# Kernel tuning notes

Measured on AMD Instinct MI355X. Metric: run time of the kernel, lower is better.

Reference implementation:

```python
import jax, jax.numpy as jnp
import numpy as np

HID = 1024
IN_DIM = 512
BATCH = 4096


def setup_inputs() -> dict:
    key = jax.random.key(0)
    ks = jax.random.split(key, 7)
    def lin(k, fan_in, fan_out):
        bound = 1.0 / np.sqrt(fan_in)
        kw, kb = jax.random.split(k)
        W = jax.random.uniform(kw, (fan_in, fan_out), jnp.float32, -bound, bound)
        b = jax.random.uniform(kb, (fan_out,), jnp.float32, -bound, bound)
        return W, b
    W_e, b_e = lin(ks[0], IN_DIM, HID)
    W_d, b_d = lin(ks[1], 4 * HID, HID)
    W_r, b_r = lin(ks[2], 3 * HID, 1)
    x = jax.random.normal(ks[3], (BATCH, IN_DIM), jnp.float32)
    return {"x": x, "W_e": W_e, "b_e": b_e, "W_d": W_d, "b_d": b_d,
            "W_r": W_r, "b_r": b_r, "steps": 12}


def reference(x, W_e, b_e, W_d, b_d, W_r, b_r, steps):
    # p: (B, h) embedded phases
    p = x @ W_e + b_e
    xp_c = jnp.cos(p)  # xp[:, :, 0]
    xp_s = jnp.sin(p)  # xp[:, :, 1]

    def step(ph, _):
        inp = jnp.concatenate([jnp.cos(ph), jnp.sin(ph), xp_c, xp_s], axis=1)  # (B, 4h)
        ph_new = ph + inp @ W_d + b_d
        return ph_new, ph_new

    ph0 = jnp.zeros((x.shape[0], W_e.shape[1]), dtype=x.dtype)
    ph, H = jax.lax.scan(step, ph0, None, length=steps)  # H: (steps, B, h)
    out = jnp.concatenate([jnp.cos(ph), jnp.sin(ph), ph], axis=1) @ W_r + b_r  # (B, 1)
    return out, H
```

## Files before the change

### kernel.cpp

```cpp
#include <hip/hip_runtime.h>
#include <hip/hip_bf16.h>
#include <math.h>

#define HID 1024
#define BATCH 4096
#define STEPS 12

typedef __attribute__((ext_vector_type(8))) short short8;
typedef __attribute__((ext_vector_type(4))) float f32x4;
typedef __attribute__((ext_vector_type(4))) unsigned short us4;
typedef unsigned short u16;

__device__ __forceinline__ u16 f2bf(float f) {
    union { float f; unsigned u; } v; v.f = f;
    unsigned r = v.u + 0x7fffu + ((v.u >> 16) & 1u);
    return (u16)(r >> 16);
}

__device__ __forceinline__ void gload_lds16(const u16* g, u16* l) {
    __builtin_amdgcn_global_load_lds(
        (const __attribute__((address_space(1))) unsigned*)g,
        (__attribute__((address_space(3))) unsigned*)l, 16, 0, 0);
}


__global__ void rm_convert_bf16(const float* __restrict__ in, u16* __restrict__ out, int n4) {
    int i = blockIdx.x * 256 + threadIdx.x;
    if (i >= n4) return;
    f32x4 v = *(const f32x4*)(in + (size_t)i * 4);
    us4 o;
    o[0] = f2bf(v[0]); o[1] = f2bf(v[1]); o[2] = f2bf(v[2]); o[3] = f2bf(v[3]);
    *(us4*)(out + (size_t)i * 4) = o;
}

__global__ void rm_transpose_bf16(const float* __restrict__ in, u16* __restrict__ out, int R, int C) {
    __shared__ float t[32][33];
    int c0 = blockIdx.x * 32, r0 = blockIdx.y * 32;
    int tx = threadIdx.x & 31, ty = threadIdx.x >> 5;
    #pragma unroll
    for (int i = 0; i < 32; i += 8)
        t[ty + i][tx] = in[(size_t)(r0 + ty + i) * C + (c0 + tx)];
    __syncthreads();
    #pragma unroll
    for (int i = 0; i < 32; i += 8)
        out[(size_t)(c0 + ty + i) * R + (r0 + tx)] = f2bf(t[tx][ty + i]);
}

__global__ void rm_w1sum(const float* __restrict__ W_d, float* __restrict__ w1sum) {
    int c  = blockIdx.x * 256 + threadIdx.x;
    int k0 = blockIdx.y * 64;
    float s = 0.f;
    for (int k = 0; k < 64; ++k) s += W_d[(size_t)(k0 + k) * HID + c];
    atomicAdd(&w1sum[c], s);
}

__global__ void rm_step0(const float* __restrict__ base, const float* __restrict__ w1sum,
                         float* __restrict__ H0, u16* __restrict__ cs) {
    int i = blockIdx.x * 256 + threadIdx.x;
    int c4 = i & 255;
    size_t r = (size_t)(i >> 8);
    f32x4 b = *(const f32x4*)(base + (size_t)i * 4);
    f32x4 w = *(const f32x4*)(w1sum + c4 * 4);
    f32x4 v = b + w;
    *(f32x4*)(H0 + (size_t)i * 4) = v;
    us4 co, so;
    #pragma unroll
    for (int j = 0; j < 4; ++j) {
        float sn, cn; __sincosf(v[j], &sn, &cn);
        co[j] = f2bf(cn); so[j] = f2bf(sn);
    }
    *(us4*)(cs + r * 2048 + c4 * 4) = co;
    *(us4*)(cs + r * 2048 + 1024 + c4 * 4) = so;
}

template<int KTOT, int LDA, int LDB, int MODE>
__global__ __launch_bounds__(256)
void rm_gemm(const u16* __restrict__ A, const u16* __restrict__ Bt,
             const float* __restrict__ bias, const float* __restrict__ base,
             const float* __restrict__ prev, float* __restrict__ out32,
             u16* __restrict__ csOut)
{
    constexpr int NT = KTOT / 64;
    __shared__ u16 sm[2][2][128 * 64];
    const int tid = threadIdx.x, lane = tid & 63, wid = tid >> 6;

    const int wg    = blockIdx.x;
    const int tileM = ((wg & 7) * 4 + ((wg >> 3) >> 3)) * 128;
    const int tileN = ((wg >> 3) & 7) * 128;

    const int srow = lane >> 3;
    const int scol = ((lane & 7) ^ srow) * 8;

    const int wr = wid >> 1, wc = wid & 1;
    const int lrow = lane & 15, lk8 = (lane >> 4) * 8;

    f32x4 acc[4][4] = {};

    auto stage = [&](int buf, int kt) {
        const int k0 = kt * 64;
        #pragma unroll
        for (int p = 0; p < 4; ++p) {
            const int chunk = p * 4 + wid;
            const int row = chunk * 8 + srow;
            gload_lds16(A  + (size_t)(tileM + row) * LDA + k0 + scol,
                        &sm[buf][0][0] + chunk * 512);
            gload_lds16(Bt + (size_t)(tileN + row) * LDB + k0 + scol,
                        &sm[buf][1][0] + chunk * 512);
        }
    };

    auto compute = [&](int buf) {
        #pragma unroll
        for (int kk = 0; kk < 64; kk += 32) {
            short8 a[4], b[4];
            #pragma unroll
            for (int m = 0; m < 4; ++m) {
                const int r = wr * 64 + m * 16 + lrow;
                a[m] = *(const short8*)&sm[buf][0][r * 64 + ((kk + lk8) ^ ((r & 7) << 3))];
            }
            #pragma unroll
            for (int n = 0; n < 4; ++n) {
                const int r = wc * 64 + n * 16 + lrow;
                b[n] = *(const short8*)&sm[buf][1][r * 64 + ((kk + lk8) ^ ((r & 7) << 3))];
            }
            #pragma unroll
            for (int m = 0; m < 4; ++m)
                #pragma unroll
                for (int n = 0; n < 4; ++n)
                    acc[m][n] = __builtin_amdgcn_mfma_f32_16x16x32_bf16(a[m], b[n], acc[m][n], 0, 0, 0);
        }
    };

    stage(0, 0);
    #pragma unroll 1
    for (int t = 0; t < NT; ++t) {
        if (t + 1 < NT) {
            stage((t + 1) & 1, t + 1);
            asm volatile("s_waitcnt vmcnt(8)" ::: "memory");
        } else {
            asm volatile("s_waitcnt vmcnt(0)" ::: "memory");
        }
        __builtin_amdgcn_s_barrier();
        asm volatile("" ::: "memory");
        compute(t & 1);
        asm volatile("s_waitcnt lgkmcnt(0)" ::: "memory");
        __builtin_amdgcn_s_barrier();
        asm volatile("" ::: "memory");
    }

    const int rbase = (lane >> 4) * 4;
    #pragma unroll
    for (int m = 0; m < 4; ++m) {
        #pragma unroll
        for (int n = 0; n < 4; ++n) {
            const int c = tileN + wc * 64 + n * 16 + (lane & 15);
            #pragma unroll
            for (int j = 0; j < 4; ++j) {
                const int r = tileM + wr * 64 + m * 16 + rbase + j;
                float v = acc[m][n][j];
                if constexpr (MODE == 2) v += base[(size_t)r * HID + c] + prev[(size_t)r * HID + c];
                else                     v += bias[c];
                if constexpr (MODE != 0) out32[(size_t)r * HID + c] = v;
                if constexpr (MODE != 1) {
                    float sn, cn;
                    __sincosf(v, &sn, &cn);
                    csOut[(size_t)r * 2048 + c]       = f2bf(cn);
                    csOut[(size_t)r * 2048 + HID + c] = f2bf(sn);
                }
            }
        }
    }
}

__global__ void rm_final(const float* __restrict__ ph, const float* __restrict__ W_r,
                         const float* __restrict__ b_r, float* __restrict__ out) {
    const int lane = threadIdx.x & 63;
    const int row  = blockIdx.x * 4 + (threadIdx.x >> 6);
    const float* p = ph + (size_t)row * HID;
    float s = 0.f;
    for (int j = lane; j < HID; j += 64) {
        float v = p[j];
        float sn, cn;
        __sincosf(v, &sn, &cn);
        s += cn * W_r[j] + sn * W_r[HID + j] + v * W_r[2 * HID + j];
    }
    #pragma unroll
    for (int off = 32; off; off >>= 1) s += __shfl_down(s, off);
    if (lane == 0) out[row] = s + b_r[0];
}

extern "C" void kernel_launch(void* const* d_in, const int* in_sizes, int n_in,
                              void* d_out, int out_size, void* d_ws, size_t ws_size,
                              hipStream_t stream) {
    const float* x   = (const float*)d_in[0];
    const float* W_e = (const float*)d_in[1];
    const float* b_e = (const float*)d_in[2];
    const float* W_d = (const float*)d_in[3];
    const float* b_d = (const float*)d_in[4];
    const float* W_r = (const float*)d_in[5];
    const float* b_r = (const float*)d_in[6];

    float* out = (float*)d_out;
    float* H   = out + BATCH;

    u16* x_bf   = (u16*)d_ws;
    u16* W_eT   = x_bf + (size_t)BATCH * 512;
    u16* W_dT   = W_eT + (size_t)HID * 512;
    u16* xp     = W_dT + (size_t)HID * 4096;
    u16* csA    = xp   + (size_t)BATCH * 2048;
    u16* csB    = csA  + (size_t)BATCH * 2048;
    float* baseB = (float*)(csB + (size_t)BATCH * 2048);
    float* w1sum = baseB + (size_t)BATCH * HID;

    rm_convert_bf16<<<(BATCH * 512 / 4 + 255) / 256, 256, 0, stream>>>(x, x_bf, BATCH * 512 / 4);
    rm_transpose_bf16<<<dim3(HID / 32, 512 / 32), 256, 0, stream>>>(W_e, W_eT, 512, HID);
    rm_transpose_bf16<<<dim3(HID / 32, 4096 / 32), 256, 0, stream>>>(W_d, W_dT, 4096, HID);
    hipMemsetAsync(w1sum, 0, HID * sizeof(float), stream);
    rm_w1sum<<<dim3(HID / 256, 16), 256, 0, stream>>>(W_d, w1sum);

    rm_gemm<512, 512, 512, 0><<<256, 256, 0, stream>>>(
        x_bf, W_eT, b_e, nullptr, nullptr, nullptr, xp);

    rm_gemm<2048, 2048, 4096, 1><<<256, 256, 0, stream>>>(
        xp, W_dT + 2048, b_d, nullptr, nullptr, baseB, nullptr);

    rm_step0<<<BATCH * HID / 4 / 256, 256, 0, stream>>>(baseB, w1sum, H, csB);

    u16* cs[2] = {csA, csB};
    for (int t = 1; t < STEPS; ++t) {
        rm_gemm<2048, 2048, 4096, 2><<<256, 256, 0, stream>>>(
            cs[t & 1], W_dT, nullptr, baseB,
            H + (size_t)(t - 1) * BATCH * HID,
            H + (size_t)t * BATCH * HID, cs[(t + 1) & 1]);
    }

    rm_final<<<BATCH / 4, 256, 0, stream>>>(H + (size_t)(STEPS - 1) * BATCH * HID, W_r, b_r, out);
}
```

Measured before the change: 425.9 us.

## Fuse recurrent steps into one persistent kernel with grid barriers and triple buffering

Replaces the per-step GEMM launches and the step0 kernel with a single persistent kernel of 256 blocks. Each block keeps its phase tile and the constant base term in registers across steps and separates steps with a global atomic grid barrier. This removes the launch gaps, the reloads of base and prev from memory, and the baseB buffer. The K-loop also moves from double to triple LDS buffering. It relies on all 256 blocks being co-resident, with one block per CU, and adds spin-wait barrier overhead.

```diff
diff --git a/kernel.cpp b/kernel.cpp
--- a/kernel.cpp
+++ b/kernel.cpp
@@ -5,6 +5,7 @@
 #define HID 1024
 #define BATCH 4096
 #define STEPS 12
+#define NBLK 256
 
 typedef __attribute__((ext_vector_type(8))) short short8;
 typedef __attribute__((ext_vector_type(4))) float f32x4;
@@ -54,47 +55,16 @@
     atomicAdd(&w1sum[c], s);
 }
 
-__global__ void rm_step0(const float* __restrict__ base, const float* __restrict__ w1sum,
-                         float* __restrict__ H0, u16* __restrict__ cs) {
-    int i = blockIdx.x * 256 + threadIdx.x;
-    int c4 = i & 255;
-    size_t r = (size_t)(i >> 8);
-    f32x4 b = *(const f32x4*)(base + (size_t)i * 4);
-    f32x4 w = *(const f32x4*)(w1sum + c4 * 4);
-    f32x4 v = b + w;
-    *(f32x4*)(H0 + (size_t)i * 4) = v;
-    us4 co, so;
-    #pragma unroll
-    for (int j = 0; j < 4; ++j) {
-        float sn, cn; __sincosf(v[j], &sn, &cn);
-        co[j] = f2bf(cn); so[j] = f2bf(sn);
-    }
-    *(us4*)(cs + r * 2048 + c4 * 4) = co;
-    *(us4*)(cs + r * 2048 + 1024 + c4 * 4) = so;
-}
-
-template<int KTOT, int LDA, int LDB, int MODE>
-__global__ __launch_bounds__(256)
-void rm_gemm(const u16* __restrict__ A, const u16* __restrict__ Bt,
-             const float* __restrict__ bias, const float* __restrict__ base,
-             const float* __restrict__ prev, float* __restrict__ out32,
-             u16* __restrict__ csOut)
+template<int NT, int LDA, int LDB>
+__device__ __forceinline__ void kloop(const u16* A, const u16* Bt,
+                                      u16 (&Asm)[3][128 * 64], u16 (&Bsm)[3][128 * 64],
+                                      f32x4 (&acc)[4][4],
+                                      int tileM, int tileN, int lane, int wid)
 {
-    constexpr int NT = KTOT / 64;
-    __shared__ u16 sm[2][2][128 * 64];
-    const int tid = threadIdx.x, lane = tid & 63, wid = tid >> 6;
-
-    const int wg    = blockIdx.x;
-    const int tileM = ((wg & 7) * 4 + ((wg >> 3) >> 3)) * 128;
-    const int tileN = ((wg >> 3) & 7) * 128;
-
     const int srow = lane >> 3;
     const int scol = ((lane & 7) ^ srow) * 8;
-
     const int wr = wid >> 1, wc = wid & 1;
     const int lrow = lane & 15, lk8 = (lane >> 4) * 8;
-
-    f32x4 acc[4][4] = {};
 
     auto stage = [&](int buf, int kt) {
         const int k0 = kt * 64;
@@ -102,13 +72,10 @@
         for (int p = 0; p < 4; ++p) {
             const int chunk = p * 4 + wid;
             const int row = chunk * 8 + srow;
-            gload_lds16(A  + (size_t)(tileM + row) * LDA + k0 + scol,
-                        &sm[buf][0][0] + chunk * 512);
-            gload_lds16(Bt + (size_t)(tileN + row) * LDB + k0 + scol,
-                        &sm[buf][1][0] + chunk * 512);
+            gload_lds16(A  + (size_t)(tileM + row) * LDA + k0 + scol, &Asm[buf][0] + chunk * 512);
+            gload_lds16(Bt + (size_t)(tileN + row) * LDB + k0 + scol, &Bsm[buf][0] + chunk * 512);
         }
     };
-
     auto compute = [&](int buf) {
         #pragma unroll
         for (int kk = 0; kk < 64; kk += 32) {
@@ -116,12 +83,12 @@
             #pragma unroll
             for (int m = 0; m < 4; ++m) {
                 const int r = wr * 64 + m * 16 + lrow;
-                a[m] = *(const short8*)&sm[buf][0][r * 64 + ((kk + lk8) ^ ((r & 7) << 3))];
+                a[m] = *(const short8*)&Asm[buf][r * 64 + ((kk + lk8) ^ ((r & 7) << 3))];
             }
             #pragma unroll
             for (int n = 0; n < 4; ++n) {
                 const int r = wc * 64 + n * 16 + lrow;
-                b[n] = *(const short8*)&sm[buf][1][r * 64 + ((kk + lk8) ^ ((r & 7) << 3))];
+                b[n] = *(const short8*)&Bsm[buf][r * 64 + ((kk + lk8) ^ ((r & 7) << 3))];
             }
             #pragma unroll
             for (int m = 0; m < 4; ++m)
@@ -132,43 +99,136 @@
     };
 
     stage(0, 0);
+    stage(1, 1);
     #pragma unroll 1
     for (int t = 0; t < NT; ++t) {
-        if (t + 1 < NT) {
-            stage((t + 1) & 1, t + 1);
+        if (t + 2 < NT) {
+            stage((t + 2) % 3, t + 2);
+            asm volatile("s_waitcnt vmcnt(16)" ::: "memory");
+        } else if (t + 1 < NT) {
             asm volatile("s_waitcnt vmcnt(8)" ::: "memory");
         } else {
             asm volatile("s_waitcnt vmcnt(0)" ::: "memory");
         }
         __builtin_amdgcn_s_barrier();
-        asm volatile("" ::: "memory");
-        compute(t & 1);
+        compute(t % 3);
         asm volatile("s_waitcnt lgkmcnt(0)" ::: "memory");
         __builtin_amdgcn_s_barrier();
-        asm volatile("" ::: "memory");
-    }
+    }
+}
+
+__global__ __launch_bounds__(256, 1)
+void rm_embed(const u16* __restrict__ A, const u16* __restrict__ Bt,
+              const float* __restrict__ bias, u16* __restrict__ csOut)
+{
+    __shared__ u16 Asm[3][128 * 64];
+    __shared__ u16 Bsm[3][128 * 64];
+    const int tid = threadIdx.x, lane = tid & 63, wid = tid >> 6;
+    const int wg = blockIdx.x, xcd = wg & 7, idx = wg >> 3;
+    const int tileM = (xcd * 4 + (idx >> 3)) * 128;
+    const int tileN = (idx & 7) * 128;
+    const int wr = wid >> 1, wc = wid & 1;
+
+    f32x4 acc[4][4] = {};
+    kloop<8, 512, 512>(A, Bt, Asm, Bsm, acc, tileM, tileN, lane, wid);
 
     const int rbase = (lane >> 4) * 4;
     #pragma unroll
-    for (int m = 0; m < 4; ++m) {
+    for (int m = 0; m < 4; ++m)
         #pragma unroll
         for (int n = 0; n < 4; ++n) {
             const int c = tileN + wc * 64 + n * 16 + (lane & 15);
             #pragma unroll
             for (int j = 0; j < 4; ++j) {
                 const int r = tileM + wr * 64 + m * 16 + rbase + j;
-                float v = acc[m][n][j];
-                if constexpr (MODE == 2) v += base[(size_t)r * HID + c] + prev[(size_t)r * HID + c];
-                else                     v += bias[c];
-                if constexpr (MODE != 0) out32[(size_t)r * HID + c] = v;
-                if constexpr (MODE != 1) {
-                    float sn, cn;
-                    __sincosf(v, &sn, &cn);
-                    csOut[(size_t)r * 2048 + c]       = f2bf(cn);
-                    csOut[(size_t)r * 2048 + HID + c] = f2bf(sn);
+                float v = acc[m][n][j] + bias[c];
+                float sn, cn; __sincosf(v, &sn, &cn);
+                csOut[(size_t)r * 2048 + c]       = f2bf(cn);
+                csOut[(size_t)r * 2048 + HID + c] = f2bf(sn);
+            }
+        }
+}
+
+__device__ __forceinline__ void gridbar(unsigned* bar, unsigned target) {
+    __syncthreads();
+    if (threadIdx.x == 0) {
+        __threadfence();
+        atomicAdd(bar, 1u);
+        while (__hip_atomic_load(bar, __ATOMIC_RELAXED, __HIP_MEMORY_SCOPE_AGENT) < target)
+            __builtin_amdgcn_s_sleep(2);
+        __threadfence();
+    }
+    __syncthreads();
+}
+
+__global__ __launch_bounds__(256, 1)
+void rm_steps(const u16* __restrict__ xp, const u16* __restrict__ W_dT,
+              const float* __restrict__ b_d, const float* __restrict__ w1sum,
+              u16* __restrict__ csA, u16* __restrict__ csB,
+              float* __restrict__ H, unsigned* __restrict__ bar)
+{
+    __shared__ u16 Asm[3][128 * 64];
+    __shared__ u16 Bsm[3][128 * 64];
+    const int tid = threadIdx.x, lane = tid & 63, wid = tid >> 6;
+    const int wg = blockIdx.x, xcd = wg & 7, idx = wg >> 3;
+    const int tileM = (xcd * 4 + (idx >> 3)) * 128;
+    const int tileN = (idx & 7) * 128;
+    const int wr = wid >> 1, wc = wid & 1;
+    const int rbase = (lane >> 4) * 4;
+
+    f32x4 acc[4][4] = {};
+    f32x4 basev[4][4];
+
+    kloop<32, 2048, 4096>(xp, W_dT + 2048, Asm, Bsm, acc, tileM, tileN, lane, wid);
+
+    #pragma unroll
+    for (int m = 0; m < 4; ++m)
+        #pragma unroll
+        for (int n = 0; n < 4; ++n) {
+            const int c = tileN + wc * 64 + n * 16 + (lane & 15);
+            const float wv = w1sum[c], bv = b_d[c];
+            #pragma unroll
+            for (int j = 0; j < 4; ++j) {
+                const int r = tileM + wr * 64 + m * 16 + rbase + j;
+                float bb = acc[m][n][j] + bv;
+                basev[m][n][j] = bb;
+                float v = bb + wv;
+                acc[m][n][j] = v;
+                H[(size_t)r * HID + c] = v;
+                float sn, cn; __sincosf(v, &sn, &cn);
+                csB[(size_t)r * 2048 + c]       = f2bf(cn);
+                csB[(size_t)r * 2048 + HID + c] = f2bf(sn);
+            }
+        }
+
+    gridbar(bar, NBLK);
+
+    #pragma unroll 1
+    for (int t = 1; t < STEPS; ++t) {
+        const u16* A   = (t & 1) ? csB : csA;
+        u16* csOut     = (t & 1) ? csA : csB;
+        kloop<32, 2048, 4096>(A, W_dT, Asm, Bsm, acc, tileM, tileN, lane, wid);
+
+        float* Ht = H + (size_t)t * BATCH * HID;
+        #pragma unroll
+        for (int m = 0; m < 4; ++m)
+            #pragma unroll
+            for (int n = 0; n < 4; ++n) {
+                const int c = tileN + wc * 64 + n * 16 + (lane & 15);
+                #pragma unroll
+                for (int j = 0; j < 4; ++j) {
+                    const int r = tileM + wr * 64 + m * 16 + rbase + j;
+                    float v = acc[m][n][j] + basev[m][n][j];
+                    acc[m][n][j] = v;
+                    Ht[(size_t)r * HID + c] = v;
+                    if (t < STEPS - 1) {
+                        float sn, cn; __sincosf(v, &sn, &cn);
+                        csOut[(size_t)r * 2048 + c]       = f2bf(cn);
+                        csOut[(size_t)r * 2048 + HID + c] = f2bf(sn);
+                    }
                 }
             }
-        }
+        if (t < STEPS - 1) gridbar(bar, (unsigned)(t + 1) * NBLK);
     }
 }
 
@@ -209,30 +269,19 @@
     u16* xp     = W_dT + (size_t)HID * 4096;
     u16* csA    = xp   + (size_t)BATCH * 2048;
     u16* csB    = csA  + (size_t)BATCH * 2048;
-    float* baseB = (float*)(csB + (size_t)BATCH * 2048);
-    float* w1sum = baseB + (size_t)BATCH * HID;
+    float* w1sum = (float*)(csB + (size_t)BATCH * 2048);
+    unsigned* bar = (unsigned*)(w1sum + HID);
 
     rm_convert_bf16<<<(BATCH * 512 / 4 + 255) / 256, 256, 0, stream>>>(x, x_bf, BATCH * 512 / 4);
     rm_transpose_bf16<<<dim3(HID / 32, 512 / 32), 256, 0, stream>>>(W_e, W_eT, 512, HID);
     rm_transpose_bf16<<<dim3(HID / 32, 4096 / 32), 256, 0, stream>>>(W_d, W_dT, 4096, HID);
     hipMemsetAsync(w1sum, 0, HID * sizeof(float), stream);
+    hipMemsetAsync(bar, 0, sizeof(unsigned), stream);
     rm_w1sum<<<dim3(HID / 256, 16), 256, 0, stream>>>(W_d, w1sum);
 
-    rm_gemm<512, 512, 512, 0><<<256, 256, 0, stream>>>(
-        x_bf, W_eT, b_e, nullptr, nullptr, nullptr, xp);
-
-    rm_gemm<2048, 2048, 4096, 1><<<256, 256, 0, stream>>>(
-        xp, W_dT + 2048, b_d, nullptr, nullptr, baseB, nullptr);
-
-    rm_step0<<<BATCH * HID / 4 / 256, 256, 0, stream>>>(baseB, w1sum, H, csB);
-
-    u16* cs[2] = {csA, csB};
-    for (int t = 1; t < STEPS; ++t) {
-        rm_gemm<2048, 2048, 4096, 2><<<256, 256, 0, stream>>>(
-            cs[t & 1], W_dT, nullptr, baseB,
-            H + (size_t)(t - 1) * BATCH * HID,
-            H + (size_t)t * BATCH * HID, cs[(t + 1) & 1]);
-    }
+    rm_embed<<<NBLK, 256, 0, stream>>>(x_bf, W_eT, b_e, xp);
+
+    rm_steps<<<NBLK, 256, 0, stream>>>(xp, W_dT, b_d, w1sum, csA, csB, H, bar);
 
     rm_final<<<BATCH / 4, 256, 0, stream>>>(H + (size_t)(STEPS - 1) * BATCH * HID, W_r, b_r, out);
 }
```

New measurement: 801.6 us. 1.88x slower.

## Triple-buffer GEMM K-loop, fuse step0 into base GEMM, skip last sincos

Applied to the files above, without the earlier changes.

Moves the GEMM main loop to a three-stage LDS ring buffer so two K-tiles are in flight ahead of compute, instead of one. Folds the step-0 elementwise kernel into the base GEMM epilogue, which now writes baseB, H0 and the cos/sin buffer directly and removes one launch plus a full read and write of baseB. Skips the cos/sin output on the last recurrent step, where nothing reads it, and changes the tile-to-block mapping to a simple row-major order. The extra buffer raises LDS use to 96KB per block with launch_bounds(256,1), which may limit occupancy.

```diff
diff --git a/kernel.cpp b/kernel.cpp
--- a/kernel.cpp
+++ b/kernel.cpp
@@ -54,47 +54,16 @@
     atomicAdd(&w1sum[c], s);
 }
 
-__global__ void rm_step0(const float* __restrict__ base, const float* __restrict__ w1sum,
-                         float* __restrict__ H0, u16* __restrict__ cs) {
-    int i = blockIdx.x * 256 + threadIdx.x;
-    int c4 = i & 255;
-    size_t r = (size_t)(i >> 8);
-    f32x4 b = *(const f32x4*)(base + (size_t)i * 4);
-    f32x4 w = *(const f32x4*)(w1sum + c4 * 4);
-    f32x4 v = b + w;
-    *(f32x4*)(H0 + (size_t)i * 4) = v;
-    us4 co, so;
-    #pragma unroll
-    for (int j = 0; j < 4; ++j) {
-        float sn, cn; __sincosf(v[j], &sn, &cn);
-        co[j] = f2bf(cn); so[j] = f2bf(sn);
-    }
-    *(us4*)(cs + r * 2048 + c4 * 4) = co;
-    *(us4*)(cs + r * 2048 + 1024 + c4 * 4) = so;
-}
-
-template<int KTOT, int LDA, int LDB, int MODE>
-__global__ __launch_bounds__(256)
-void rm_gemm(const u16* __restrict__ A, const u16* __restrict__ Bt,
-             const float* __restrict__ bias, const float* __restrict__ base,
-             const float* __restrict__ prev, float* __restrict__ out32,
-             u16* __restrict__ csOut)
+template<int NT, int LDA, int LDB>
+__device__ __forceinline__ void kloop(const u16* A, const u16* Bt,
+                                      u16 (&Asm)[3][128 * 64], u16 (&Bsm)[3][128 * 64],
+                                      f32x4 (&acc)[4][4],
+                                      int tileM, int tileN, int lane, int wid)
 {
-    constexpr int NT = KTOT / 64;
-    __shared__ u16 sm[2][2][128 * 64];
-    const int tid = threadIdx.x, lane = tid & 63, wid = tid >> 6;
-
-    const int wg    = blockIdx.x;
-    const int tileM = ((wg & 7) * 4 + ((wg >> 3) >> 3)) * 128;
-    const int tileN = ((wg >> 3) & 7) * 128;
-
     const int srow = lane >> 3;
     const int scol = ((lane & 7) ^ srow) * 8;
-
     const int wr = wid >> 1, wc = wid & 1;
     const int lrow = lane & 15, lk8 = (lane >> 4) * 8;
-
-    f32x4 acc[4][4] = {};
 
     auto stage = [&](int buf, int kt) {
         const int k0 = kt * 64;
@@ -102,13 +71,10 @@
         for (int p = 0; p < 4; ++p) {
             const int chunk = p * 4 + wid;
             const int row = chunk * 8 + srow;
-            gload_lds16(A  + (size_t)(tileM + row) * LDA + k0 + scol,
-                        &sm[buf][0][0] + chunk * 512);
-            gload_lds16(Bt + (size_t)(tileN + row) * LDB + k0 + scol,
-                        &sm[buf][1][0] + chunk * 512);
+            gload_lds16(A  + (size_t)(tileM + row) * LDA + k0 + scol, &Asm[buf][0] + chunk * 512);
+            gload_lds16(Bt + (size_t)(tileN + row) * LDB + k0 + scol, &Bsm[buf][0] + chunk * 512);
         }
     };
-
     auto compute = [&](int buf) {
         #pragma unroll
         for (int kk = 0; kk < 64; kk += 32) {
@@ -116,12 +82,12 @@
             #pragma unroll
             for (int m = 0; m < 4; ++m) {
                 const int r = wr * 64 + m * 16 + lrow;
-                a[m] = *(const short8*)&sm[buf][0][r * 64 + ((kk + lk8) ^ ((r & 7) << 3))];
+                a[m] = *(const short8*)&Asm[buf][r * 64 + ((kk + lk8) ^ ((r & 7) << 3))];
             }
             #pragma unroll
             for (int n = 0; n < 4; ++n) {
                 const int r = wc * 64 + n * 16 + lrow;
-                b[n] = *(const short8*)&sm[buf][1][r * 64 + ((kk + lk8) ^ ((r & 7) << 3))];
+                b[n] = *(const short8*)&Bsm[buf][r * 64 + ((kk + lk8) ^ ((r & 7) << 3))];
             }
             #pragma unroll
             for (int m = 0; m < 4; ++m)
@@ -132,21 +98,41 @@
     };
 
     stage(0, 0);
+    stage(1, 1);
     #pragma unroll 1
     for (int t = 0; t < NT; ++t) {
-        if (t + 1 < NT) {
-            stage((t + 1) & 1, t + 1);
+        if (t + 2 < NT) {
+            stage((t + 2) % 3, t + 2);
+            asm volatile("s_waitcnt vmcnt(16)" ::: "memory");
+        } else if (t + 1 < NT) {
             asm volatile("s_waitcnt vmcnt(8)" ::: "memory");
         } else {
             asm volatile("s_waitcnt vmcnt(0)" ::: "memory");
         }
         __builtin_amdgcn_s_barrier();
-        asm volatile("" ::: "memory");
-        compute(t & 1);
+        compute(t % 3);
         asm volatile("s_waitcnt lgkmcnt(0)" ::: "memory");
         __builtin_amdgcn_s_barrier();
-        asm volatile("" ::: "memory");
-    }
+    }
+}
+
+template<int KTOT, int LDA, int LDB, int MODE>
+__global__ __launch_bounds__(256, 1)
+void rm_gemm(const u16* __restrict__ A, const u16* __restrict__ Bt,
+             const float* __restrict__ bias, const float* __restrict__ w1sum,
+             float* __restrict__ baseB, const float* __restrict__ prev,
+             float* __restrict__ out32, u16* __restrict__ csOut)
+{
+    __shared__ u16 Asm[3][128 * 64];
+    __shared__ u16 Bsm[3][128 * 64];
+    const int tid = threadIdx.x, lane = tid & 63, wid = tid >> 6;
+    const int wg = blockIdx.x;
+    const int tileN = (wg & 7) * 128;
+    const int tileM = (wg >> 3) * 128;
+    const int wr = wid >> 1, wc = wid & 1;
+
+    f32x4 acc[4][4] = {};
+    kloop<KTOT / 64, LDA, LDB>(A, Bt, Asm, Bsm, acc, tileM, tileN, lane, wid);
 
     const int rbase = (lane >> 4) * 4;
     #pragma unroll
@@ -158,10 +144,18 @@
             for (int j = 0; j < 4; ++j) {
                 const int r = tileM + wr * 64 + m * 16 + rbase + j;
                 float v = acc[m][n][j];
-                if constexpr (MODE == 2) v += base[(size_t)r * HID + c] + prev[(size_t)r * HID + c];
-                else                     v += bias[c];
-                if constexpr (MODE != 0) out32[(size_t)r * HID + c] = v;
-                if constexpr (MODE != 1) {
+                if constexpr (MODE == 2) {
+                    v += baseB[(size_t)r * HID + c] + prev[(size_t)r * HID + c];
+                    out32[(size_t)r * HID + c] = v;
+                } else if constexpr (MODE == 1) {
+                    float bb = v + bias[c];
+                    baseB[(size_t)r * HID + c] = bb;
+                    v = bb + w1sum[c];
+                    out32[(size_t)r * HID + c] = v;
+                } else {
+                    v += bias[c];
+                }
+                if (MODE == 0 || MODE == 1 || csOut != nullptr) {
                     float sn, cn;
                     __sincosf(v, &sn, &cn);
                     csOut[(size_t)r * 2048 + c]       = f2bf(cn);
@@ -219,19 +213,18 @@
     rm_w1sum<<<dim3(HID / 256, 16), 256, 0, stream>>>(W_d, w1sum);
 
     rm_gemm<512, 512, 512, 0><<<256, 256, 0, stream>>>(
-        x_bf, W_eT, b_e, nullptr, nullptr, nullptr, xp);
+        x_bf, W_eT, b_e, nullptr, nullptr, nullptr, nullptr, xp);
 
     rm_gemm<2048, 2048, 4096, 1><<<256, 256, 0, stream>>>(
-        xp, W_dT + 2048, b_d, nullptr, nullptr, baseB, nullptr);
-
-    rm_step0<<<BATCH * HID / 4 / 256, 256, 0, stream>>>(baseB, w1sum, H, csB);
+        xp, W_dT + 2048, b_d, w1sum, baseB, nullptr, H, csB);
 
     u16* cs[2] = {csA, csB};
     for (int t = 1; t < STEPS; ++t) {
         rm_gemm<2048, 2048, 4096, 2><<<256, 256, 0, stream>>>(
-            cs[t & 1], W_dT, nullptr, baseB,
+            cs[t & 1], W_dT, nullptr, nullptr, baseB,
             H + (size_t)(t - 1) * BATCH * HID,
-            H + (size_t)t * BATCH * HID, cs[(t + 1) & 1]);
+            H + (size_t)t * BATCH * HID,
+            (t < STEPS - 1) ? cs[(t + 1) & 1] : nullptr);
     }
 
     rm_final<<<BATCH / 4, 256, 0, stream>>>(H + (size_t)(STEPS - 1) * BATCH * HID, W_r, b_r, out);
```

Measured after the change: 664.3 us. 56.0% more time.
